# Optimization experiments

Hardware: AMD Instinct MI355X
Metric: run time of the kernel (lower is better)

Reference implementation:

```python
import jax, jax.numpy as jnp
import numpy as np

H_LSTM = 80          # span-encoder LSTM hidden
SPAN_DIM = 4 * H_LSTM  # 320
ADU_DIM = 256        # han_out_size
HEADS = 3
HAN_HID = 256
CTX_DIM = 200


def lstm(x, W_ih, W_hh, b, reverse=False):
    # x: [T, B, In] -> hidden states [T, B, H]; torch gate order i,f,g,o
    H = W_hh.shape[1]
    B = x.shape[1]

    def step(carry, xt):
        h, c = carry
        z = xt @ W_ih.T + h @ W_hh.T + b
        i, f, g, o = jnp.split(z, 4, axis=-1)
        c = jax.nn.sigmoid(f) * c + jax.nn.sigmoid(i) * jnp.tanh(g)
        h = jax.nn.sigmoid(o) * jnp.tanh(c)
        return (h, c), h

    init = (jnp.zeros((B, H), x.dtype), jnp.zeros((B, H), x.dtype))
    _, hs = jax.lax.scan(step, init, x, reverse=reverse)
    return hs


def span_rep(seq, spans):
    # seq [L, 2H], spans [..., 2] -> [..., 4H]
    f, bwd = seq[:, :H_LSTM], seq[:, H_LSTM:]
    i, j = spans[..., 0], spans[..., 1]
    fi1, fj = f[i - 1], f[j]
    bi, bj1 = bwd[i], bwd[j + 1]
    return jnp.concatenate([fj - fi1, bi - bj1, fi1, bj1], axis=-1)


def gat_metapath(h, src, dst, emask, W, a_l, a_r, bias):
    # single-metapath GATConv (dgl semantics): h [A, Din], W [K, Din, D]
    A = h.shape[0]
    hp = jnp.einsum('ad,kdo->ako', h, W)  # [A,K,D]
    e = jax.nn.leaky_relu(jnp.einsum('eko,ko->ek', hp[src], a_l)
                          + jnp.einsum('eko,ko->ek', hp[dst], a_r), 0.2)
    e = jnp.where(emask[:, None], e, -1e9)
    m = jax.ops.segment_max(e, dst, num_segments=A)           # [A,K]
    ex = jnp.where(emask[:, None], jnp.exp(e - m[dst]), 0.0)
    den = jax.ops.segment_sum(ex, dst, num_segments=A)
    alpha = ex / jnp.maximum(den[dst], 1e-9)                  # edge softmax per dst
    out = jax.ops.segment_sum(alpha[:, :, None] * hp[src], dst, num_segments=A)
    out = jax.nn.elu(out + bias)                              # [A,K,D]
    return out.reshape(A, -1)                                 # [A, K*D]


def attn_pool(feats, vals, mask, W1, b1, W2, b2):
    # tiny MLP -> Softmax over axis 0 over the kept (masked) set
    s = jnp.maximum(feats @ W1 + b1, 0.0) @ W2 + b2           # [N,1]
    s = jnp.where(mask[:, None], s, -1e9)
    a = jnp.where(mask[:, None], jax.nn.softmax(s, axis=0), 0.0)
    out = (a * vals).sum(0)
    return jnp.where(mask.any(), out, jnp.zeros_like(out))


def _forward(token_embed, info_scores,
             Wih_f, Whh_f, b_f, Wih_b, Whh_b, b_b,
             W_gat, a_l, a_r, b_gat, W_sem, b_sem, q_sem, W_pred, b_pred,
             W_adu1, b_adu1, W_adu2, b_adu2,
             W_inn1, b_inn1, W_inn2, b_inn2,
             W_int1, b_int1, W_int2, b_int2,
             Wih_c, Whh_c, b_c,
             comment_spans, adu_spans, adu_masks, local_masks,
             inner_src, inner_dst, inner_rel, inner_mask,
             inter_src, inter_dst, inter_rel, inter_mask):
    # bidirectional span encoder over frozen LF token embeddings
    x = token_embed.transpose(1, 0, 2)                        # [L, C, 768]
    hf = lstm(x, Wih_f, Whh_f, b_f)
    hb = lstm(x, Wih_b, Whh_b, b_b, reverse=True)
    span_enc = jnp.concatenate([hf, hb], -1).transpose(1, 0, 2)  # [C, L, 2H]

    def per_comment(seq, cspan, aspans, amask, lmask,
                    isrc, idst, irel, imask_e,
                    tsrc, tdst, trel, tmask_e, info):
        cemb = span_rep(seq, cspan)                           # [320]
        adus = span_rep(seq, aspans) * amask[:, None]         # [A, 320]
        A = adus.shape[0]
        # meta-paths: inner Attack, inner Support, inter AttackedBy(rev), inter SupportedBy(rev)
        srcs = jnp.stack([isrc, isrc, tdst, tdst])
        dsts = jnp.stack([idst, idst, tsrc, tsrc])
        masks = jnp.stack([imask_e & (irel == 0), imask_e & (irel == 1),
                           tmask_e & (trel == 0), tmask_e & (trel == 1)])
        z = jax.vmap(gat_metapath, in_axes=(None, 0, 0, 0, 0, 0, 0, 0))(
            adus, srcs, dsts, masks, W_gat, a_l, a_r, b_gat)  # [4, A, K*D]
        # semantic attention across meta-paths (masked mean over real nodes)
        w = jnp.tanh(z @ W_sem + b_sem) @ q_sem               # [4, A]
        w = (w * amask[None, :]).sum(1) / jnp.maximum(amask.sum(), 1)
        beta = jax.nn.softmax(w)                              # [4]
        zfin = jnp.einsum('m,mad->ad', beta, z)               # [A, K*D]
        adu_embeds = zfin @ W_pred + b_pred                   # [A, 256]
        # ADU attention pooling over locally-used ADUs
        feats = jnp.concatenate(
            [jnp.broadcast_to(cemb, (A, SPAN_DIM)), adu_embeds], -1)
        attended_adu = attn_pool(feats, adu_embeds, amask & lmask,
                                 W_adu1, b_adu1, W_adu2, b_adu2)

        def pair_attend(se, de, rel, me, W1, b1, W2, b2):
            # relation lut: Attack(0)->[0,1], Support(1)->[1,0]
            onehot = jnp.stack([rel, 1 - rel], -1).astype(adu_embeds.dtype)
            pe = jnp.concatenate([adu_embeds[se], adu_embeds[de], onehot], -1)  # [E,514]
            fp = jnp.concatenate(
                [jnp.broadcast_to(cemb, (pe.shape[0], SPAN_DIM)), pe], -1)
            return attn_pool(fp, pe, me, W1, b1, W2, b2)

        attended_inner = pair_attend(isrc, idst, irel, imask_e,
                                     W_inn1, b_inn1, W_inn2, b_inn2)
        # revert_inter_post_relations=True: embed = cat(emb[pair1], emb[pair0], rel)
        attended_inter = pair_attend(tdst, tsrc, trel, tmask_e,
                                     W_int1, b_int1, W_int2, b_int2)
        return jnp.concatenate([attended_adu, attended_inner, attended_inter,
                                info, cemb])                  # [1608]

    wo_ctx = jax.vmap(per_comment)(span_enc, comment_spans, adu_spans, adu_masks,
                                   local_masks, inner_src, inner_dst, inner_rel,
                                   inner_mask, inter_src, inter_dst, inter_rel,
                                   inter_mask, info_scores)   # [C, 1608]
    # comment compressor LSTM along the comment sequence (batch = 1)
    ctx = lstm(wo_ctx[:, None, :], Wih_c, Whh_c, b_c)[:, 0, :]  # [C, 200]
    return jnp.concatenate([ctx, wo_ctx], -1)                 # [C, 1808]


def setup_inputs():
    C, L, A, E, INFO = 64, 1024, 32, 48, 4
    key = jax.random.key(0)
    ks = iter(jax.random.split(key, 64))
    rng = np.random.default_rng(0)

    def u(shape):  # uniform init as in _weight_init, scaled for stability
        return jax.random.uniform(next(ks), shape, jnp.float32, -0.1, 0.1)

    token_embed = jax.random.normal(next(ks), (C, L, 768), jnp.float32)
    info_scores = jax.random.normal(next(ks), (C, INFO), jnp.float32)
    ci = rng.integers(1, L // 2, C)
    cj = rng.integers(L // 2, L - 2, C)
    comment_spans = jnp.stack([jnp.asarray(ci), jnp.asarray(cj)], 1).astype(jnp.int32)
    ai = rng.integers(1, L - 40, (C, A))
    adu_spans = jnp.stack([jnp.asarray(ai), jnp.asarray(ai + rng.integers(1, 30, (C, A)))], -1).astype(jnp.int32)
    adu_masks = jnp.ones((C, A), jnp.bool_)
    local_masks = jnp.asarray(rng.integers(0, 2, (C, A)) > 0)
    ei = lambda hi, shp: jnp.asarray(rng.integers(0, hi, shp), jnp.int32)
    eb = lambda shp: jnp.asarray(rng.integers(0, 2, shp) > 0)
    inp = dict(token_embed=token_embed, info_scores=info_scores,
               comment_spans=comment_spans, adu_spans=adu_spans,
               adu_masks=adu_masks, local_masks=local_masks,
               inner_src=ei(A, (C, E)), inner_dst=ei(A, (C, E)),
               inner_rel=ei(2, (C, E)), inner_mask=eb((C, E)),
               inter_src=ei(A, (C, E)), inter_dst=ei(A, (C, E)),
               inter_rel=ei(2, (C, E)), inter_mask=eb((C, E)))
    D_WO = SPAN_DIM + ADU_DIM * 5 + 4 + INFO  # 1608
    params = dict(
        Wih_f=u((4 * H_LSTM, 768)), Whh_f=u((4 * H_LSTM, H_LSTM)), b_f=u((4 * H_LSTM,)),
        Wih_b=u((4 * H_LSTM, 768)), Whh_b=u((4 * H_LSTM, H_LSTM)), b_b=u((4 * H_LSTM,)),
        W_gat=u((4, HEADS, SPAN_DIM, HAN_HID)), a_l=u((4, HEADS, HAN_HID)),
        a_r=u((4, HEADS, HAN_HID)), b_gat=u((4, HEADS, HAN_HID)),
        W_sem=u((HEADS * HAN_HID, 128)), b_sem=u((128,)), q_sem=u((128,)),
        W_pred=u((HEADS * HAN_HID, ADU_DIM)), b_pred=u((ADU_DIM,)),
        W_adu1=u((SPAN_DIM + ADU_DIM, 16)), b_adu1=u((16,)), W_adu2=u((16, 1)), b_adu2=u((1,)),
        W_inn1=u((SPAN_DIM + 2 * ADU_DIM + 2, 16)), b_inn1=u((16,)), W_inn2=u((16, 1)), b_inn2=u((1,)),
        W_int1=u((SPAN_DIM + 2 * ADU_DIM + 2, 16)), b_int1=u((16,)), W_int2=u((16, 1)), b_int2=u((1,)),
        Wih_c=u((4 * CTX_DIM, D_WO)), Whh_c=u((4 * CTX_DIM, CTX_DIM)), b_c=u((4 * CTX_DIM,)))
    inp.update(params)
    return inp


def reference(token_embed, info_scores,
              Wih_f, Whh_f, b_f, Wih_b, Whh_b, b_b,
              W_gat, a_l, a_r, b_gat, W_sem, b_sem, q_sem, W_pred, b_pred,
              W_adu1, b_adu1, W_adu2, b_adu2,
              W_inn1, b_inn1, W_inn2, b_inn2,
              W_int1, b_int1, W_int2, b_int2,
              Wih_c, Whh_c, b_c,
              comment_spans, adu_spans, adu_masks, local_masks,
              inner_src, inner_dst, inner_rel, inner_mask,
              inter_src, inter_dst, inter_rel, inter_mask):
    return _forward(token_embed, info_scores,
                    Wih_f, Whh_f, b_f, Wih_b, Whh_b, b_b,
                    W_gat, a_l, a_r, b_gat, W_sem, b_sem, q_sem, W_pred, b_pred,
                    W_adu1, b_adu1, W_adu2, b_adu2,
                    W_inn1, b_inn1, W_inn2, b_inn2,
                    W_int1, b_int1, W_int2, b_int2,
                    Wih_c, Whh_c, b_c,
                    comment_spans, adu_spans, adu_masks, local_masks,
                    inner_src, inner_dst, inner_rel, inner_mask,
                    inter_src, inter_dst, inter_rel, inter_mask)
```

## Files before the change

kernel.cpp:

```cpp
#include <hip/hip_runtime.h>
#include <hip/hip_bf16.h>
#include <hip/hip_fp16.h>
#include <stdint.h>

typedef unsigned int u32;
typedef unsigned short u16;
typedef __attribute__((ext_vector_type(8))) short short8;
typedef __attribute__((ext_vector_type(4))) float f32x4;
typedef _Float16 half2v __attribute__((ext_vector_type(2)));

#if defined(__has_builtin)
#if __has_builtin(__builtin_amdgcn_fdot2)
#define HAVE_FDOT2 1
#endif
#endif

__device__ __forceinline__ float bf2f_u(u32 lo16) { return __uint_as_float(lo16 << 16); }
__device__ __forceinline__ u32 f2bf_bits(float x) {
  u32 u = __float_as_uint(x);
  return (u + 0x7fffu + ((u >> 16) & 1u)) >> 16;
}
__device__ __forceinline__ u32 pk2bf(float x, float y) {
  return f2bf_bits(x) | (f2bf_bits(y) << 16);
}
__device__ __forceinline__ u32 pk2bf_tr(float x, float y) {
  return (__float_as_uint(y) & 0xffff0000u) | (__float_as_uint(x) >> 16);
}
__device__ __forceinline__ u32 pkh(float x, float y) {
  return (u32)__half_as_ushort(__float2half(x)) |
         ((u32)__half_as_ushort(__float2half(y)) << 16);
}
__device__ __forceinline__ float dot2h(u32 w, u32 h, float acc) {
#ifdef HAVE_FDOT2
  return __builtin_amdgcn_fdot2(__builtin_bit_cast(half2v, w), __builtin_bit_cast(half2v, h),
                                acc, false);
#else
  union { u32 u; __half2 h2; } uw, uh;
  uw.u = w; uh.u = h;
  float2 wf = __half22float2(uw.h2);
  float2 hf = __half22float2(uh.h2);
  return acc + wf.x * hf.x + wf.y * hf.y;
#endif
}
__device__ __forceinline__ float sigf(float x) { return 1.0f / (1.0f + __expf(-x)); }
__device__ __forceinline__ float tanhf_fast(float x) {
  float ax = fabsf(x);
  float e = __expf(-2.0f * ax);
  float t = (1.0f - e) / (1.0f + e);
  return x < 0.0f ? -t : t;
}
__device__ __forceinline__ float eluf(float x) { return x > 0.0f ? x : __expf(x) - 1.0f; }
__device__ __forceinline__ float lreluf(float x) { return x > 0.0f ? x : 0.2f * x; }

__device__ __forceinline__ int maskmode(const void* am) { return (*(const u32*)am) > 0xFFu; }
__device__ __forceinline__ int ldmask(const void* p, int i, int mb) {
  return mb ? (int)((const unsigned char*)p)[i] : ((const int*)p)[i];
}

__global__ void k_marker(float* out) { out[0] = 12345.0f; }

__global__ void k_prep(const float* __restrict__ Wgat, const float* __restrict__ al,
                       const float* __restrict__ ar, float* __restrict__ alproj,
                       float* __restrict__ arproj) {
  int idx = blockIdx.x * 256 + threadIdx.x;
  if (idx >= 3840) return;
  int mk = idx / 320, d = idx % 320;
  const float* wrow = Wgat + ((size_t)mk * 320 + d) * 256;
  const float* alp = al + mk * 256;
  const float* arp = ar + mk * 256;
  float sa = 0.f, sb = 0.f;
  for (int o = 0; o < 256; ++o) {
    float w = wrow[o];
    sa += w * alp[o];
    sb += w * arp[o];
  }
  alproj[idx] = sa;
  arproj[idx] = sb;
}

__global__ void k_pack(const float* __restrict__ whhc, uint4* __restrict__ wt4) {
  int idx = blockIdx.x * 256 + threadIdx.x;
  if (idx >= 20000) return;
  int k4 = idx / 800, r = idx % 800;
  const float* p = whhc + r * 200 + k4 * 8;
  wt4[idx] = (uint4){pkh(p[0], p[1]), pkh(p[2], p[3]), pkh(p[4], p[5]), pkh(p[6], p[7])};
}

__global__ __launch_bounds__(256) void k_gemm_in(
    const float* __restrict__ emb, const float* __restrict__ Wf, const float* __restrict__ Wb,
    const float* __restrict__ biasf, const float* __restrict__ biasb, float* __restrict__ Z) {
  __shared__ u16 Albs[128 * 40];
  __shared__ u16 Blbs[128 * 40];
  __shared__ float bias_l[128];
  const int tid = threadIdx.x;
  const int n0 = blockIdx.x * 128;
  const int m0 = blockIdx.y * 128;

  if (tid < 128) {
    int ng = n0 + tid;
    bias_l[tid] = (ng < 320) ? biasf[ng] : biasb[ng - 320];
  }

  const int srow = tid >> 1, shalf = tid & 1;
  const float* asrc = emb + (size_t)(m0 + srow) * 768 + shalf * 16;
  const int ngb = n0 + srow;
  const float* bsrc =
      ((ngb < 320) ? (Wf + (size_t)ngb * 768) : (Wb + (size_t)(ngb - 320) * 768)) + shalf * 16;
  u32* aw = (u32*)&Albs[srow * 40 + shalf * 16];
  u32* bw = (u32*)&Blbs[srow * 40 + shalf * 16];

  const int lane = tid & 63;
  const int lr = lane & 15, sub = lane >> 4;
  const int wv = tid >> 6, wm = wv >> 1, wn = wv & 1;
  const u16* abase = &Albs[(wm * 64 + lr) * 40 + sub * 8];
  const u16* bbase = &Blbs[(wn * 64 + lr) * 40 + sub * 8];

  f32x4 acc[4][4];
#pragma unroll
  for (int i = 0; i < 4; ++i)
#pragma unroll
    for (int j = 0; j < 4; ++j) acc[i][j] = (f32x4)(0.f);

  float4 a0, a1, a2, a3, b0, b1, b2, b3;
  u32 pra[8], prb[8];
  a0 = *(const float4*)(asrc + 0); a1 = *(const float4*)(asrc + 4);
  a2 = *(const float4*)(asrc + 8); a3 = *(const float4*)(asrc + 12);
  b0 = *(const float4*)(bsrc + 0); b1 = *(const float4*)(bsrc + 4);
  b2 = *(const float4*)(bsrc + 8); b3 = *(const float4*)(bsrc + 12);
  pra[0] = pk2bf_tr(a0.x, a0.y); pra[1] = pk2bf_tr(a0.z, a0.w);
  pra[2] = pk2bf_tr(a1.x, a1.y); pra[3] = pk2bf_tr(a1.z, a1.w);
  pra[4] = pk2bf_tr(a2.x, a2.y); pra[5] = pk2bf_tr(a2.z, a2.w);
  pra[6] = pk2bf_tr(a3.x, a3.y); pra[7] = pk2bf_tr(a3.z, a3.w);
  prb[0] = pk2bf_tr(b0.x, b0.y); prb[1] = pk2bf_tr(b0.z, b0.w);
  prb[2] = pk2bf_tr(b1.x, b1.y); prb[3] = pk2bf_tr(b1.z, b1.w);
  prb[4] = pk2bf_tr(b2.x, b2.y); prb[5] = pk2bf_tr(b2.z, b2.w);
  prb[6] = pk2bf_tr(b3.x, b3.y); prb[7] = pk2bf_tr(b3.z, b3.w);

  for (int it = 0; it < 24; ++it) {
    __syncthreads();
#pragma unroll
    for (int q = 0; q < 8; ++q) { aw[q] = pra[q]; bw[q] = prb[q]; }
    __syncthreads();
    const bool more = (it + 1 < 24);
    if (more) {
      const int k0 = (it + 1) * 32;
      a0 = *(const float4*)(asrc + k0); a1 = *(const float4*)(asrc + k0 + 4);
      a2 = *(const float4*)(asrc + k0 + 8); a3 = *(const float4*)(asrc + k0 + 12);
      b0 = *(const float4*)(bsrc + k0); b1 = *(const float4*)(bsrc + k0 + 4);
      b2 = *(const float4*)(bsrc + k0 + 8); b3 = *(const float4*)(bsrc + k0 + 12);
    }
    short8 bfr[4];
#pragma unroll
    for (int nf = 0; nf < 4; ++nf) bfr[nf] = *(const short8*)(bbase + nf * 640);
#pragma unroll
    for (int mf = 0; mf < 4; ++mf) {
      short8 af = *(const short8*)(abase + mf * 640);
#pragma unroll
      for (int nf = 0; nf < 4; ++nf)
        acc[mf][nf] = __builtin_amdgcn_mfma_f32_16x16x32_bf16(af, bfr[nf], acc[mf][nf], 0, 0, 0);
    }
    if (more) {
      pra[0] = pk2bf_tr(a0.x, a0.y); pra[1] = pk2bf_tr(a0.z, a0.w);
      pra[2] = pk2bf_tr(a1.x, a1.y); pra[3] = pk2bf_tr(a1.z, a1.w);
      pra[4] = pk2bf_tr(a2.x, a2.y); pra[5] = pk2bf_tr(a2.z, a2.w);
      pra[6] = pk2bf_tr(a3.x, a3.y); pra[7] = pk2bf_tr(a3.z, a3.w);
      prb[0] = pk2bf_tr(b0.x, b0.y); prb[1] = pk2bf_tr(b0.z, b0.w);
      prb[2] = pk2bf_tr(b1.x, b1.y); prb[3] = pk2bf_tr(b1.z, b1.w);
      prb[4] = pk2bf_tr(b2.x, b2.y); prb[5] = pk2bf_tr(b2.z, b2.w);
      prb[6] = pk2bf_tr(b3.x, b3.y); prb[7] = pk2bf_tr(b3.z, b3.w);
    }
  }

#pragma unroll
  for (int mf = 0; mf < 4; ++mf) {
#pragma unroll
    for (int nf = 0; nf < 4; ++nf) {
      int col = wn * 64 + nf * 16 + lr;
      float bias = bias_l[col];
      size_t mrow = (size_t)m0 + wm * 64 + mf * 16 + sub * 4;
#pragma unroll
      for (int j = 0; j < 4; ++j)
        Z[(mrow + j) * 640 + n0 + col] = acc[mf][nf][j] + bias;
    }
  }
}

__global__ __launch_bounds__(320, 1) void k_lstm_tok(const float* __restrict__ Z,
                                                     const float* __restrict__ Whhf,
                                                     const float* __restrict__ Whhb,
                                                     float* __restrict__ hf,
                                                     float* __restrict__ hb) {
  __shared__ uint2 wq[20 * 320];
  __shared__ alignas(16) u32 hpk[40];
  __shared__ float zbuf[320];
  const int tid = threadIdx.x;
  const int c = blockIdx.x >> 1;
  const int dir = blockIdx.x & 1;
  const float* Whh = dir ? Whhb : Whhf;
  float* hout = dir ? hb : hf;

  for (int idx = tid; idx < 20 * 320; idx += 320) {
    int k4 = idx / 320, r = idx % 320;
    const float* p = Whh + (size_t)r * 80 + k4 * 4;
    wq[idx] = (uint2){pkh(p[0], p[1]), pkh(p[2], p[3])};
  }
  if (tid < 40) hpk[tid] = 0;
  __syncthreads();

  const int j = tid;
  const uint2* wcol = wq + j;
  uint2 wv0 = wcol[0], wv1 = wcol[320], wv2 = wcol[640], wv3 = wcol[960];
  uint2 wv4 = wcol[1280], wv5 = wcol[1600], wv6 = wcol[1920], wv7 = wcol[2240];
  uint2 wv8 = wcol[2560], wv9 = wcol[2880], wv10 = wcol[3200], wv11 = wcol[3520];
  uint2 wv12 = wcol[3840], wv13 = wcol[4160], wv14 = wcol[4480], wv15 = wcol[4800];
  uint2 wv16 = wcol[5120], wv17 = wcol[5440], wv18 = wcol[5760], wv19 = wcol[6080];
  asm volatile("" : "+v"(wv0.x), "+v"(wv0.y), "+v"(wv1.x), "+v"(wv1.y), "+v"(wv2.x),
                    "+v"(wv2.y), "+v"(wv3.x), "+v"(wv3.y), "+v"(wv4.x), "+v"(wv4.y),
                    "+v"(wv5.x), "+v"(wv5.y), "+v"(wv6.x), "+v"(wv6.y), "+v"(wv7.x),
                    "+v"(wv7.y), "+v"(wv8.x), "+v"(wv8.y), "+v"(wv9.x), "+v"(wv9.y));
  asm volatile("" : "+v"(wv10.x), "+v"(wv10.y), "+v"(wv11.x), "+v"(wv11.y), "+v"(wv12.x),
                    "+v"(wv12.y), "+v"(wv13.x), "+v"(wv13.y), "+v"(wv14.x), "+v"(wv14.y),
                    "+v"(wv15.x), "+v"(wv15.y), "+v"(wv16.x), "+v"(wv16.y), "+v"(wv17.x),
                    "+v"(wv17.y), "+v"(wv18.x), "+v"(wv18.y), "+v"(wv19.x), "+v"(wv19.y));

  const int sgn = dir ? -1 : 1;
  const int t0 = dir ? 1023 : 0;
  const float* zb = Z + (size_t)c * 1024 * 640 + dir * 320 + j;
  float zc = zb[(size_t)t0 * 640];
  float zn = zb[(size_t)(t0 + sgn) * 640];
  float cst = 0.f;

  for (int t = 0; t < 1024; ++t) {
    const int tt = t0 + sgn * t;
    float zp = 0.f;
    if (t + 2 < 1024) zp = zb[(size_t)(t0 + sgn * (t + 2)) * 640];
    float a0 = zc, a1 = 0.f, a2 = 0.f, a3 = 0.f;
    {
      uint4 h0 = *(const uint4*)&hpk[0];
      a0 = dot2h(wv0.x, h0.x, a0); a1 = dot2h(wv0.y, h0.y, a1);
      a2 = dot2h(wv1.x, h0.z, a2); a3 = dot2h(wv1.y, h0.w, a3);
      uint4 h1 = *(const uint4*)&hpk[4];
      a0 = dot2h(wv2.x, h1.x, a0); a1 = dot2h(wv2.y, h1.y, a1);
      a2 = dot2h(wv3.x, h1.z, a2); a3 = dot2h(wv3.y, h1.w, a3);
      uint4 h2 = *(const uint4*)&hpk[8];
      a0 = dot2h(wv4.x, h2.x, a0); a1 = dot2h(wv4.y, h2.y, a1);
      a2 = dot2h(wv5.x, h2.z, a2); a3 = dot2h(wv5.y, h2.w, a3);
      uint4 h3 = *(const uint4*)&hpk[12];
      a0 = dot2h(wv6.x, h3.x, a0); a1 = dot2h(wv6.y, h3.y, a1);
      a2 = dot2h(wv7.x, h3.z, a2); a3 = dot2h(wv7.y, h3.w, a3);
      uint4 h4 = *(const uint4*)&hpk[16];
      a0 = dot2h(wv8.x, h4.x, a0); a1 = dot2h(wv8.y, h4.y, a1);
      a2 = dot2h(wv9.x, h4.z, a2); a3 = dot2h(wv9.y, h4.w, a3);
      uint4 h5 = *(const uint4*)&hpk[20];
      a0 = dot2h(wv10.x, h5.x, a0); a1 = dot2h(wv10.y, h5.y, a1);
      a2 = dot2h(wv11.x, h5.z, a2); a3 = dot2h(wv11.y, h5.w, a3);
      uint4 h6 = *(const uint4*)&hpk[24];
      a0 = dot2h(wv12.x, h6.x, a0); a1 = dot2h(wv12.y, h6.y, a1);
      a2 = dot2h(wv13.x, h6.z, a2); a3 = dot2h(wv13.y, h6.w, a3);
      uint4 h7 = *(const uint4*)&hpk[28];
      a0 = dot2h(wv14.x, h7.x, a0); a1 = dot2h(wv14.y, h7.y, a1);
      a2 = dot2h(wv15.x, h7.z, a2); a3 = dot2h(wv15.y, h7.w, a3);
      uint4 h8 = *(const uint4*)&hpk[32];
      a0 = dot2h(wv16.x, h8.x, a0); a1 = dot2h(wv16.y, h8.y, a1);
      a2 = dot2h(wv17.x, h8.z, a2); a3 = dot2h(wv17.y, h8.w, a3);
      uint4 h9 = *(const uint4*)&hpk[36];
      a0 = dot2h(wv18.x, h9.x, a0); a1 = dot2h(wv18.y, h9.y, a1);
      a2 = dot2h(wv19.x, h9.z, a2); a3 = dot2h(wv19.y, h9.w, a3);
    }
    zbuf[j] = (a0 + a1) + (a2 + a3);
    __syncthreads();
    if (j < 80) {
      float iv = sigf(zbuf[j]);
      float fv = sigf(zbuf[80 + j]);
      float gv = tanhf_fast(zbuf[160 + j]);
      float ov = sigf(zbuf[240 + j]);
      cst = fv * cst + iv * gv;
      float h = ov * tanhf_fast(cst);
      ((u16*)hpk)[j] = __half_as_ushort(__float2half(h));
      hout[((size_t)c * 1024 + tt) * 80 + j] = h;
    }
    zc = zn; zn = zp;
    __syncthreads();
  }
}

__device__ __forceinline__ float span_val(const float* __restrict__ hf,
                                          const float* __restrict__ hb, int c, int i, int j,
                                          int d) {
  size_t base = (size_t)c * 1024 * 80;
  if (d < 80) return hf[base + (size_t)j * 80 + d] - hf[base + (size_t)(i - 1) * 80 + d];
  if (d < 160) return hb[base + (size_t)i * 80 + (d - 80)] - hb[base + (size_t)(j + 1) * 80 + (d - 80)];
  if (d < 240) return hf[base + (size_t)(i - 1) * 80 + (d - 160)];
  return hb[base + (size_t)(j + 1) * 80 + (d - 240)];
}

__global__ __launch_bounds__(256) void k_span(const float* __restrict__ hf,
                                              const float* __restrict__ hb,
                                              const int* __restrict__ cspan,
                                              const int* __restrict__ aspan,
                                              const void* __restrict__ amask,
                                              float* __restrict__ adus, float* __restrict__ cembo) {
  const int c = blockIdx.x, tid = threadIdx.x;
  const int mb = maskmode(amask);
  int ci = cspan[c * 2], cj = cspan[c * 2 + 1];
  for (int d = tid; d < 320; d += 256) cembo[c * 320 + d] = span_val(hf, hb, c, ci, cj, d);
  for (int idx = tid; idx < 32 * 320; idx += 256) {
    int a = idx / 320, d = idx % 320;
    float v = 0.f;
    if (ldmask(amask, c * 32 + a, mb)) {
      int ai = aspan[(c * 32 + a) * 2], aj = aspan[(c * 32 + a) * 2 + 1];
      v = span_val(hf, hb, c, ai, aj, d);
    }
    adus[(size_t)c * 10240 + idx] = v;
  }
}

__global__ __launch_bounds__(256) void k_gat(
    const float* __restrict__ adus_ws, const float* __restrict__ alproj,
    const float* __restrict__ arproj, const float* __restrict__ Wgat,
    const float* __restrict__ bgat, const int* __restrict__ isrc, const int* __restrict__ idst,
    const int* __restrict__ irel, const void* __restrict__ imask, const int* __restrict__ tsrc,
    const int* __restrict__ tdst, const int* __restrict__ trel, const void* __restrict__ tmask,
    const void* __restrict__ amdet, float* __restrict__ zgat) {
  __shared__ float adus_l[32][321];
  __shared__ float Wst[16][64];
  __shared__ float hp_t[32][66];
  __shared__ float sl_l[96], sr_l[96];
  __shared__ float e_l[144], alpha_l[144], mx_l[96], den_l[96];
  __shared__ int src_l[48], dst_l[48], valid_l[48];
  const int c = blockIdx.x >> 2, m = blockIdx.x & 3;
  const int tid = threadIdx.x;
  const int mb = maskmode(amdet);

  if (tid < 48) {
    int e = tid, s, d, r, mk;
    if (m < 2) {
      s = isrc[c * 48 + e]; d = idst[c * 48 + e]; r = irel[c * 48 + e];
      mk = ldmask(imask, c * 48 + e, mb);
    } else {
      s = tdst[c * 48 + e]; d = tsrc[c * 48 + e]; r = trel[c * 48 + e];
      mk = ldmask(tmask, c * 48 + e, mb);
    }
    src_l[e] = s; dst_l[e] = d; valid_l[e] = (mk != 0) && (r == (m & 1));
  }
  for (int idx = tid; idx < 32 * 320; idx += 256)
    adus_l[idx / 320][idx % 320] = adus_ws[(size_t)c * 10240 + idx];
  __syncthreads();

  if (tid < 96) {
    int a = tid & 31, k = tid >> 5;
    const float* alp = alproj + (m * 3 + k) * 320;
    const float* arp = arproj + (m * 3 + k) * 320;
    float sa = 0.f, sb = 0.f;
    for (int d = 0; d < 320; ++d) {
      float v = adus_l[a][d];
      sa += v * alp[d];
      sb += v * arp[d];
    }
    sl_l[a * 3 + k] = sa;
    sr_l[a * 3 + k] = sb;
  }
  __syncthreads();
  if (tid < 144) {
    int e = tid % 48, k = tid / 48;
    float v = -1e30f;
    if (valid_l[e]) v = lreluf(sl_l[src_l[e] * 3 + k] + sr_l[dst_l[e] * 3 + k]);
    e_l[e * 3 + k] = v;
  }
  __syncthreads();
  if (tid < 96) {
    int a = tid & 31, k = tid >> 5;
    float mx = -1e30f;
    for (int e = 0; e < 48; ++e)
      if (valid_l[e] && dst_l[e] == a) mx = fmaxf(mx, e_l[e * 3 + k]);
    float den = 0.f;
    for (int e = 0; e < 48; ++e)
      if (valid_l[e] && dst_l[e] == a) den += __expf(e_l[e * 3 + k] - mx);
    mx_l[a * 3 + k] = mx;
    den_l[a * 3 + k] = den;
  }
  __syncthreads();
  if (tid < 144) {
    int e = tid % 48, k = tid / 48;
    float v = 0.f;
    if (valid_l[e]) {
      int d = dst_l[e];
      v = __expf(e_l[e * 3 + k] - mx_l[d * 3 + k]) / fmaxf(den_l[d * 3 + k], 1e-9f);
    }
    alpha_l[e * 3 + k] = v;
  }
  __syncthreads();

  const int ag = tid >> 3, og = tid & 7;
  for (int k = 0; k < 3; ++k) {
    for (int ot = 0; ot < 4; ++ot) {
      float acc[8];
#pragma unroll
      for (int i = 0; i < 8; ++i) acc[i] = 0.f;
      for (int dt = 0; dt < 320; dt += 16) {
        {
          int dd = tid >> 4, oq = (tid & 15) * 4;
          const float* p = Wgat + ((size_t)((m * 3 + k) * 320 + dt + dd)) * 256 + ot * 64 + oq;
          float4 v = *(const float4*)p;
          Wst[dd][oq + 0] = v.x;
          Wst[dd][oq + 1] = v.y;
          Wst[dd][oq + 2] = v.z;
          Wst[dd][oq + 3] = v.w;
        }
        __syncthreads();
#pragma unroll
        for (int dd = 0; dd < 16; ++dd) {
          float av = adus_l[ag][dt + dd];
          const float4 w0 = *(const float4*)(&Wst[dd][og * 8]);
          const float4 w1 = *(const float4*)(&Wst[dd][og * 8 + 4]);
          acc[0] += av * w0.x; acc[1] += av * w0.y; acc[2] += av * w0.z; acc[3] += av * w0.w;
          acc[4] += av * w1.x; acc[5] += av * w1.y; acc[6] += av * w1.z; acc[7] += av * w1.w;
        }
        __syncthreads();
      }
#pragma unroll
      for (int i = 0; i < 8; ++i) hp_t[ag][og * 8 + i] = acc[i];
      __syncthreads();
      float oacc[8];
#pragma unroll
      for (int i = 0; i < 8; ++i) oacc[i] = 0.f;
      for (int e = 0; e < 48; ++e) {
        if (valid_l[e] && dst_l[e] == ag) {
          float alv = alpha_l[e * 3 + k];
          int s = src_l[e];
#pragma unroll
          for (int i = 0; i < 8; ++i) oacc[i] += alv * hp_t[s][og * 8 + i];
        }
      }
#pragma unroll
      for (int i = 0; i < 8; ++i) {
        int o = ot * 64 + og * 8 + i;
        float v = eluf(oacc[i] + bgat[(m * 3 + k) * 256 + o]);
        zgat[((size_t)(c * 4 + m) * 32 + ag) * 768 + k * 256 + o] = v;
      }
      __syncthreads();
    }
  }
}

__global__ __launch_bounds__(256) void k_sem(const float* __restrict__ zgat,
                                             const float* __restrict__ Wsem,
                                             const float* __restrict__ bsem,
                                             const float* __restrict__ qsem,
                                             const void* __restrict__ amask,
                                             float* __restrict__ wsem) {
  __shared__ float Wst[64][128];
  __shared__ float zl[32][64];
  __shared__ float wred[256];
  __shared__ float war[32];
  const int c = blockIdx.x >> 2, m = blockIdx.x & 3;
  const int tid = threadIdx.x;
  const int mb = maskmode(amask);
  const int a = tid >> 3, hg = tid & 7;
  float acc[16];
#pragma unroll
  for (int i = 0; i < 16; ++i) acc[i] = 0.f;
  const float* zbase = zgat + (size_t)(c * 4 + m) * 32 * 768;
  for (int jt = 0; jt < 768; jt += 64) {
    for (int l = 0; l < 8; ++l) {
      int f4 = l * 256 + tid;
      int row = f4 >> 5, c4 = (f4 & 31) * 4;
      *(float4*)&Wst[row][c4] = *(const float4*)(Wsem + (size_t)(jt + row) * 128 + c4);
    }
    for (int l = 0; l < 2; ++l) {
      int f4 = l * 256 + tid;
      int row = f4 >> 4, c4 = (f4 & 15) * 4;
      *(float4*)&zl[row][c4] = *(const float4*)(zbase + (size_t)row * 768 + jt + c4);
    }
    __syncthreads();
    for (int j = 0; j < 64; ++j) {
      float zv = zl[a][j];
      const float* wp = &Wst[j][hg * 16];
#pragma unroll
      for (int i = 0; i < 16; ++i) acc[i] += zv * wp[i];
    }
    __syncthreads();
  }
  float wp_ = 0.f;
#pragma unroll
  for (int i = 0; i < 16; ++i) {
    int h = hg * 16 + i;
    wp_ += tanhf_fast(acc[i] + bsem[h]) * qsem[h];
  }
  wred[tid] = wp_;
  __syncthreads();
  if (tid < 32) {
    float s = 0.f;
    for (int q = 0; q < 8; ++q) s += wred[tid * 8 + q];
    war[tid] = s;
  }
  __syncthreads();
  if (tid == 0) {
    float s = 0.f;
    int cnt = 0;
    for (int aa = 0; aa < 32; ++aa)
      if (ldmask(amask, c * 32 + aa, mb)) { s += war[aa]; cnt++; }
    wsem[c * 4 + m] = s / (float)(cnt > 1 ? cnt : 1);
  }
}

__global__ __launch_bounds__(256) void k_comment(
    const float* __restrict__ zgat, const float* __restrict__ wsem,
    const float* __restrict__ cemb_ws, const float* __restrict__ Wpred,
    const float* __restrict__ bpred, const float* __restrict__ Wadu1,
    const float* __restrict__ badu1, const float* __restrict__ Wadu2,
    const float* __restrict__ badu2, const float* __restrict__ Winn1,
    const float* __restrict__ binn1, const float* __restrict__ Winn2,
    const float* __restrict__ binn2, const float* __restrict__ Wint1,
    const float* __restrict__ bint1, const float* __restrict__ Wint2,
    const float* __restrict__ bint2, const float* __restrict__ info,
    const void* __restrict__ amask, const void* __restrict__ lmask,
    const int* __restrict__ isrc, const int* __restrict__ idst,
    const int* __restrict__ irel, const void* __restrict__ imask, const int* __restrict__ tsrc,
    const int* __restrict__ tdst, const int* __restrict__ trel, const void* __restrict__ tmask,
    float* __restrict__ woctx, float* __restrict__ dout) {
  __shared__ float zf[32][133];
  __shared__ float ae[32][257];
  __shared__ float cemb_l[320];
  __shared__ float beta_l[4];
  __shared__ float pred_l[48][16];
  __shared__ float sE[48], alE[48];
  __shared__ int seL[48], deL[48], relL[48], mskL[48];
  __shared__ float wredA[256];
  __shared__ float sA[32], alA[32];
  __shared__ int mskA[32];
  const int c = blockIdx.x, tid = threadIdx.x;
  const int mb = maskmode(amask);

  if (tid == 0) {
    float w0 = wsem[c * 4], w1 = wsem[c * 4 + 1], w2 = wsem[c * 4 + 2], w3 = wsem[c * 4 + 3];
    float mx = fmaxf(fmaxf(w0, w1), fmaxf(w2, w3));
    float e0 = __expf(w0 - mx), e1 = __expf(w1 - mx), e2 = __expf(w2 - mx), e3 = __expf(w3 - mx);
    float s = e0 + e1 + e2 + e3;
    beta_l[0] = e0 / s; beta_l[1] = e1 / s; beta_l[2] = e2 / s; beta_l[3] = e3 / s;
  }
  for (int d = tid; d < 320; d += 256) cemb_l[d] = cemb_ws[c * 320 + d];
  __syncthreads();

  const int ag = tid >> 5;
  const int og = tid & 31;
  float acc[4][8];
#pragma unroll
  for (int i = 0; i < 4; ++i)
#pragma unroll
    for (int j = 0; j < 8; ++j) acc[i][j] = 0.f;
  const float b0 = beta_l[0], b1 = beta_l[1], b2 = beta_l[2], b3 = beta_l[3];
  const float* zc0 = zgat + (size_t)(c * 4 + 0) * 32 * 768;
  const float* zc1 = zgat + (size_t)(c * 4 + 1) * 32 * 768;
  const float* zc2 = zgat + (size_t)(c * 4 + 2) * 32 * 768;
  const float* zc3 = zgat + (size_t)(c * 4 + 3) * 32 * 768;
  for (int jt = 0; jt < 768; jt += 128) {
    for (int l = 0; l < 16; ++l) {
      int idx = l * 256 + tid;
      int a = idx >> 7, j = idx & 127;
      size_t off = (size_t)a * 768 + jt + j;
      zf[a][j] = b0 * zc0[off] + b1 * zc1[off] + b2 * zc2[off] + b3 * zc3[off];
    }
    __syncthreads();
    for (int j = 0; j < 128; ++j) {
      const float* wp = Wpred + (size_t)(jt + j) * 256 + og * 8;
      float4 w0v = *(const float4*)wp;
      float4 w1v = *(const float4*)(wp + 4);
      float w8[8] = {w0v.x, w0v.y, w0v.z, w0v.w, w1v.x, w1v.y, w1v.z, w1v.w};
      float z0 = zf[ag * 4 + 0][j], z1 = zf[ag * 4 + 1][j];
      float z2 = zf[ag * 4 + 2][j], z3 = zf[ag * 4 + 3][j];
#pragma unroll
      for (int jj = 0; jj < 8; ++jj) {
        acc[0][jj] += z0 * w8[jj];
        acc[1][jj] += z1 * w8[jj];
        acc[2][jj] += z2 * w8[jj];
        acc[3][jj] += z3 * w8[jj];
      }
    }
    __syncthreads();
  }
#pragma unroll
  for (int i = 0; i < 4; ++i)
#pragma unroll
    for (int jj = 0; jj < 8; ++jj)
      ae[ag * 4 + i][og * 8 + jj] = acc[i][jj] + bpred[og * 8 + jj];
  __syncthreads();

  {
    const int a = tid >> 3, hg = tid & 7;
    float sacc = 0.f;
    for (int hh = 0; hh < 2; ++hh) {
      int h = hg * 2 + hh;
      float d = badu1[h];
      for (int dd = 0; dd < 320; ++dd) d += cemb_l[dd] * Wadu1[dd * 16 + h];
      for (int dd = 0; dd < 256; ++dd) d += ae[a][dd] * Wadu1[(320 + dd) * 16 + h];
      sacc += fmaxf(d, 0.f) * Wadu2[h];
    }
    wredA[tid] = sacc;
  }
  __syncthreads();
  if (tid < 32) {
    float s = badu2[0];
    for (int q = 0; q < 8; ++q) s += wredA[tid * 8 + q];
    sA[tid] = s;
    mskA[tid] = (ldmask(amask, c * 32 + tid, mb) != 0) && (ldmask(lmask, c * 32 + tid, mb) != 0);
  }
  __syncthreads();
  if (tid == 0) {
    float mx = -1e30f;
    int any = 0;
    for (int a = 0; a < 32; ++a)
      if (mskA[a]) { any = 1; mx = fmaxf(mx, sA[a]); }
    float s = 0.f;
    for (int a = 0; a < 32; ++a) {
      float v = mskA[a] ? __expf(sA[a] - mx) : 0.f;
      alA[a] = v;
      s += v;
    }
    if (any)
      for (int a = 0; a < 32; ++a) alA[a] /= s;
  }
  __syncthreads();
  {
    int o = tid;
    float v = 0.f;
    for (int a = 0; a < 32; ++a) v += alA[a] * ae[a][o];
    woctx[c * 1608 + o] = v;
    dout[(size_t)c * 1808 + 200 + o] = v;
  }
  __syncthreads();

  for (int pp = 0; pp < 2; ++pp) {
    const float *W1, *b1v, *W2, *b2v;
    const int *seP, *deP, *relP;
    const void* mskP;
    int outoff;
    if (pp == 0) {
      W1 = Winn1; b1v = binn1; W2 = Winn2; b2v = binn2;
      seP = isrc; deP = idst; relP = irel; mskP = imask; outoff = 256;
    } else {
      W1 = Wint1; b1v = bint1; W2 = Wint2; b2v = bint2;
      seP = tdst; deP = tsrc; relP = trel; mskP = tmask; outoff = 770;
    }
    if (tid < 48) {
      seL[tid] = seP[c * 48 + tid];
      deL[tid] = deP[c * 48 + tid];
      relL[tid] = relP[c * 48 + tid];
      mskL[tid] = (ldmask(mskP, c * 48 + tid, mb) != 0);
    }
    __syncthreads();
    for (int u = tid; u < 768; u += 256) {
      int e = u >> 4, h = u & 15;
      int se = seL[e], de = deL[e];
      float rel = (float)relL[e];
      float d = b1v[h];
      for (int dd = 0; dd < 320; ++dd) d += cemb_l[dd] * W1[dd * 16 + h];
      for (int dd = 0; dd < 256; ++dd) d += ae[se][dd] * W1[(320 + dd) * 16 + h];
      for (int dd = 0; dd < 256; ++dd) d += ae[de][dd] * W1[(576 + dd) * 16 + h];
      d += rel * W1[832 * 16 + h] + (1.f - rel) * W1[833 * 16 + h];
      pred_l[e][h] = fmaxf(d, 0.f) * W2[h];
    }
    __syncthreads();
    if (tid < 48) {
      float s = b2v[0];
      for (int h = 0; h < 16; ++h) s += pred_l[tid][h];
      sE[tid] = s;
    }
    __syncthreads();
    if (tid == 0) {
      float mx = -1e30f;
      int any = 0;
      for (int e = 0; e < 48; ++e)
        if (mskL[e]) { any = 1; mx = fmaxf(mx, sE[e]); }
      float s = 0.f;
      for (int e = 0; e < 48; ++e) {
        float v = mskL[e] ? __expf(sE[e] - mx) : 0.f;
        alE[e] = v;
        s += v;
      }
      if (any)
        for (int e = 0; e < 48; ++e) alE[e] /= s;
    }
    __syncthreads();
    for (int dim = tid; dim < 514; dim += 256) {
      float v = 0.f;
      for (int e = 0; e < 48; ++e) {
        float alv = alE[e];
        float pe;
        if (dim < 256) pe = ae[seL[e]][dim];
        else if (dim < 512) pe = ae[deL[e]][dim - 256];
        else if (dim == 512) pe = (float)relL[e];
        else pe = 1.f - (float)relL[e];
        v += alv * pe;
      }
      woctx[c * 1608 + outoff + dim] = v;
      dout[(size_t)c * 1808 + 200 + outoff + dim] = v;
    }
    __syncthreads();
  }

  if (tid < 4) {
    float v = info[c * 4 + tid];
    woctx[c * 1608 + 1284 + tid] = v;
    dout[(size_t)c * 1808 + 200 + 1284 + tid] = v;
  }
  for (int d = tid; d < 320; d += 256) {
    float v = cemb_l[d];
    woctx[c * 1608 + 1288 + d] = v;
    dout[(size_t)c * 1808 + 200 + 1288 + d] = v;
  }
}

__global__ __launch_bounds__(256) void k_ctx_in(const float* __restrict__ woctx,
                                                const float* __restrict__ Wihc,
                                                const float* __restrict__ bc,
                                                float* __restrict__ xc) {
  __shared__ float woc[64][133];
  __shared__ float Wst[8][128];
  const int r0 = blockIdx.x * 8;
  const int tid = threadIdx.x;
  const int t = tid & 63, rg = tid >> 6;
  float a0 = 0.f, a1 = 0.f;
  for (int d0 = 0; d0 < 1608; d0 += 128) {
    int jn = 1608 - d0;
    if (jn > 128) jn = 128;
    for (int l = 0; l < 32; ++l) {
      int idx = l * 256 + tid;
      int tt = idx >> 7, j = idx & 127;
      woc[tt][j] = (j < jn) ? woctx[(size_t)tt * 1608 + d0 + j] : 0.f;
    }
    {
      int rr = tid >> 5, jb = tid & 31;
      for (int q = 0; q < 4; ++q) {
        int jj = jb * 4 + q;
        Wst[rr][jj] = (jj < jn) ? Wihc[(size_t)(r0 + rr) * 1608 + d0 + jj] : 0.f;
      }
    }
    __syncthreads();
    for (int j = 0; j < 128; ++j) {
      float x = woc[t][j];
      a0 += x * Wst[rg * 2 + 0][j];
      a1 += x * Wst[rg * 2 + 1][j];
    }
    __syncthreads();
  }
  int r = r0 + rg * 2;
  xc[t * 800 + r] = a0 + bc[r];
  xc[t * 800 + r + 1] = a1 + bc[r + 1];
}

__global__ __launch_bounds__(832) void k_ctx_rec(const float* __restrict__ xc,
                                                 const uint4* __restrict__ wt4,
                                                 float* __restrict__ dout) {
  __shared__ alignas(16) u32 hl2[100];
  __shared__ float zc[800];
  const int tid = threadIdx.x;
  if (tid < 100) hl2[tid] = 0;
  float cst = 0.f;
  __syncthreads();
  for (int t = 0; t < 64; ++t) {
    if (tid < 800) {
      float a0 = xc[t * 800 + tid], a1 = 0.f, a2 = 0.f, a3 = 0.f;
#pragma unroll 5
      for (int k4 = 0; k4 < 25; ++k4) {
        uint4 wv = wt4[(size_t)k4 * 800 + tid];
        uint4 hq = *(const uint4*)&hl2[k4 * 4];
        a0 = dot2h(wv.x, hq.x, a0);
        a1 = dot2h(wv.y, hq.y, a1);
        a2 = dot2h(wv.z, hq.z, a2);
        a3 = dot2h(wv.w, hq.w, a3);
      }
      zc[tid] = (a0 + a1) + (a2 + a3);
    }
    __syncthreads();
    if (tid < 200) {
      float iv = sigf(zc[tid]);
      float fv = sigf(zc[200 + tid]);
      float gv = tanhf_fast(zc[400 + tid]);
      float ov = sigf(zc[600 + tid]);
      cst = fv * cst + iv * gv;
      float h = ov * tanhf_fast(cst);
      ((u16*)hl2)[tid] = __half_as_ushort(__float2half(h));
      dout[(size_t)t * 1808 + tid] = h;
    }
    __syncthreads();
  }
}

extern "C" void kernel_launch(void* const* d_in, const int* in_sizes, int n_in, void* d_out,
                              int out_size, void* d_ws, size_t ws_size, hipStream_t stream) {
  const float* emb = (const float*)d_in[0];
  const float* info = (const float*)d_in[1];
  const int* cspan = (const int*)d_in[2];
  const int* aspan = (const int*)d_in[3];
  const void* amask = d_in[4];
  const void* lmask = d_in[5];
  const int* isrc = (const int*)d_in[6];
  const int* idst = (const int*)d_in[7];
  const int* irel = (const int*)d_in[8];
  const void* imask = d_in[9];
  const int* tsrc = (const int*)d_in[10];
  const int* tdst = (const int*)d_in[11];
  const int* trel = (const int*)d_in[12];
  const void* tmask = d_in[13];
  const float* Wihf = (const float*)d_in[14];
  const float* Whhf = (const float*)d_in[15];
  const float* bfv = (const float*)d_in[16];
  const float* Wihb = (const float*)d_in[17];
  const float* Whhb = (const float*)d_in[18];
  const float* bbv = (const float*)d_in[19];
  const float* Wgat = (const float*)d_in[20];
  const float* al = (const float*)d_in[21];
  const float* ar = (const float*)d_in[22];
  const float* bgat = (const float*)d_in[23];
  const float* Wsem = (const float*)d_in[24];
  const float* bsem = (const float*)d_in[25];
  const float* qsem = (const float*)d_in[26];
  const float* Wpred = (const float*)d_in[27];
  const float* bpred = (const float*)d_in[28];
  const float* Wadu1 = (const float*)d_in[29];
  const float* badu1 = (const float*)d_in[30];
  const float* Wadu2 = (const float*)d_in[31];
  const float* badu2 = (const float*)d_in[32];
  const float* Winn1 = (const float*)d_in[33];
  const float* binn1 = (const float*)d_in[34];
  const float* Winn2 = (const float*)d_in[35];
  const float* binn2 = (const float*)d_in[36];
  const float* Wint1 = (const float*)d_in[37];
  const float* bint1 = (const float*)d_in[38];
  const float* Wint2 = (const float*)d_in[39];
  const float* bint2 = (const float*)d_in[40];
  const float* Wihc = (const float*)d_in[41];
  const float* Whhc = (const float*)d_in[42];
  const float* bc = (const float*)d_in[43];
  float* out = (float*)d_out;
  float* ws = (float*)d_ws;

  const size_t OFF_Z = 0;
  const size_t OFF_HF = OFF_Z + (size_t)65536 * 640;
  const size_t OFF_HB = OFF_HF + (size_t)64 * 1024 * 80;
  const size_t OFF_ZG = OFF_HB + (size_t)64 * 1024 * 80;
  const size_t OFF_AD = OFF_ZG + (size_t)64 * 4 * 32 * 768;
  const size_t OFF_CE = OFF_AD + (size_t)64 * 32 * 320;
  const size_t OFF_WS4 = OFF_CE + 64 * 320;
  const size_t OFF_ALP = OFF_WS4 + 256;
  const size_t OFF_ARP = OFF_ALP + 3840;
  const size_t OFF_WO = OFF_ARP + 3840;
  const size_t OFF_XC = OFF_WO + (size_t)64 * 1608;
  const size_t OFF_WT = OFF_XC + (size_t)64 * 800;
  const size_t TOTAL = OFF_WT + 80000;

  if (n_in < 44 || ws_size < TOTAL * sizeof(float)) {
    k_marker<<<1, 1, 0, stream>>>(out);
    return;
  }

  k_prep<<<15, 256, 0, stream>>>(Wgat, al, ar, ws + OFF_ALP, ws + OFF_ARP);
  k_pack<<<79, 256, 0, stream>>>(Whhc, (uint4*)(ws + OFF_WT));
  dim3 g1(5, 512);
  k_gemm_in<<<g1, 256, 0, stream>>>(emb, Wihf, Wihb, bfv, bbv, ws + OFF_Z);
  k_lstm_tok<<<128, 320, 0, stream>>>(ws + OFF_Z, Whhf, Whhb, ws + OFF_HF, ws + OFF_HB);
  k_span<<<64, 256, 0, stream>>>(ws + OFF_HF, ws + OFF_HB, cspan, aspan, amask, ws + OFF_AD,
                                 ws + OFF_CE);
  k_gat<<<256, 256, 0, stream>>>(ws + OFF_AD, ws + OFF_ALP, ws + OFF_ARP, Wgat, bgat, isrc, idst,
                                 irel, imask, tsrc, tdst, trel, tmask, amask, ws + OFF_ZG);
  k_sem<<<256, 256, 0, stream>>>(ws + OFF_ZG, Wsem, bsem, qsem, amask, ws + OFF_WS4);
  k_comment<<<64, 256, 0, stream>>>(ws + OFF_ZG, ws + OFF_WS4, ws + OFF_CE, Wpred, bpred, Wadu1,
                                    badu1, Wadu2, badu2, Winn1, binn1, Winn2, binn2, Wint1, bint1,
                                    Wint2, bint2, info, amask, lmask, isrc, idst, irel, imask,
                                    tsrc, tdst, trel, tmask, ws + OFF_WO, out);
  k_ctx_in<<<100, 256, 0, stream>>>(ws + OFF_WO, Wihc, bc, ws + OFF_XC);
  k_ctx_rec<<<1, 832, 0, stream>>>(ws + OFF_XC, (const uint4*)(ws + OFF_WT), out);
}
```

Measured before the change: 1.849 ms.

## Prepack GEMM inputs to bf16 and make LSTM step use shuffles with double-buffered state

Adds separate kernels that convert the token embeddings and input weights to bf16 once, plus a GEMM variant that loads those packed operands directly. The variant runs only when the workspace is large enough. The token LSTM now assigns the four gates of each hidden unit to adjacent lanes, gathers them with wave shuffles, and double-buffers the packed hidden state. This drops one of the two block barriers per timestep. The costs are an extra pass over the full embedding tensor and a larger workspace requirement.

```diff
diff --git a/kernel.cpp b/kernel.cpp
--- a/kernel.cpp
+++ b/kernel.cpp
@@ -86,6 +86,25 @@
   wt4[idx] = (uint4){pkh(p[0], p[1]), pkh(p[2], p[3]), pkh(p[4], p[5]), pkh(p[6], p[7])};
 }
 
+__global__ void k_packemb(const float* __restrict__ emb, u32* __restrict__ dst) {
+  const float4* s = (const float4*)emb;
+  uint2* d = (uint2*)dst;
+  const int n = 12582912;
+  for (int i = blockIdx.x * blockDim.x + threadIdx.x; i < n; i += gridDim.x * blockDim.x) {
+    float4 v = s[i];
+    d[i] = (uint2){pk2bf_tr(v.x, v.y), pk2bf_tr(v.z, v.w)};
+  }
+}
+
+__global__ void k_packw(const float* __restrict__ Wf, const float* __restrict__ Wb,
+                        u32* __restrict__ dst) {
+  int idx = blockIdx.x * 256 + threadIdx.x;
+  if (idx >= 245760) return;
+  int n = idx / 384, q = (idx % 384) * 2;
+  const float* src = (n < 320) ? (Wf + (size_t)n * 768) : (Wb + (size_t)(n - 320) * 768);
+  dst[idx] = pk2bf_tr(src[q], src[q + 1]);
+}
+
 __global__ __launch_bounds__(256) void k_gemm_in(
     const float* __restrict__ emb, const float* __restrict__ Wf, const float* __restrict__ Wb,
     const float* __restrict__ biasf, const float* __restrict__ biasb, float* __restrict__ Z) {
@@ -100,7 +119,6 @@
     int ng = n0 + tid;
     bias_l[tid] = (ng < 320) ? biasf[ng] : biasb[ng - 320];
   }
-
   const int srow = tid >> 1, shalf = tid & 1;
   const float* asrc = emb + (size_t)(m0 + srow) * 768 + shalf * 16;
   const int ngb = n0 + srow;
@@ -170,7 +188,73 @@
       prb[6] = pk2bf_tr(b3.x, b3.y); prb[7] = pk2bf_tr(b3.z, b3.w);
     }
   }
-
+#pragma unroll
+  for (int mf = 0; mf < 4; ++mf) {
+#pragma unroll
+    for (int nf = 0; nf < 4; ++nf) {
+      int col = wn * 64 + nf * 16 + lr;
+      float bias = bias_l[col];
+      size_t mrow = (size_t)m0 + wm * 64 + mf * 16 + sub * 4;
+#pragma unroll
+      for (int j = 0; j < 4; ++j)
+        Z[(mrow + j) * 640 + n0 + col] = acc[mf][nf][j] + bias;
+    }
+  }
+}
+
+__global__ __launch_bounds__(256) void k_gemm_in2(
+    const u32* __restrict__ ebf, const u32* __restrict__ wbf, const float* __restrict__ biasf,
+    const float* __restrict__ biasb, float* __restrict__ Z) {
+  __shared__ u16 Albs[128 * 40];
+  __shared__ u16 Blbs[128 * 40];
+  __shared__ float bias_l[128];
+  const int tid = threadIdx.x;
+  const int n0 = blockIdx.x * 128;
+  const int m0 = blockIdx.y * 128;
+
+  if (tid < 128) {
+    int ng = n0 + tid;
+    bias_l[tid] = (ng < 320) ? biasf[ng] : biasb[ng - 320];
+  }
+  const int srow = tid >> 1, shalf = tid & 1;
+  const uint4* ea = (const uint4*)ebf + (size_t)(m0 + srow) * 96 + shalf * 2;
+  const uint4* eb = (const uint4*)wbf + (size_t)(n0 + srow) * 96 + shalf * 2;
+  uint4* aw4 = (uint4*)&Albs[srow * 40 + shalf * 16];
+  uint4* bw4 = (uint4*)&Blbs[srow * 40 + shalf * 16];
+
+  const int lane = tid & 63;
+  const int lr = lane & 15, sub = lane >> 4;
+  const int wv = tid >> 6, wm = wv >> 1, wn = wv & 1;
+  const u16* abase = &Albs[(wm * 64 + lr) * 40 + sub * 8];
+  const u16* bbase = &Blbs[(wn * 64 + lr) * 40 + sub * 8];
+
+  f32x4 acc[4][4];
+#pragma unroll
+  for (int i = 0; i < 4; ++i)
+#pragma unroll
+    for (int j = 0; j < 4; ++j) acc[i][j] = (f32x4)(0.f);
+
+  uint4 pa0 = ea[0], pa1 = ea[1], pb0 = eb[0], pb1 = eb[1];
+  for (int it = 0; it < 24; ++it) {
+    __syncthreads();
+    aw4[0] = pa0; aw4[1] = pa1;
+    bw4[0] = pb0; bw4[1] = pb1;
+    __syncthreads();
+    if (it + 1 < 24) {
+      pa0 = ea[(it + 1) * 4]; pa1 = ea[(it + 1) * 4 + 1];
+      pb0 = eb[(it + 1) * 4]; pb1 = eb[(it + 1) * 4 + 1];
+    }
+    short8 bfr[4];
+#pragma unroll
+    for (int nf = 0; nf < 4; ++nf) bfr[nf] = *(const short8*)(bbase + nf * 640);
+#pragma unroll
+    for (int mf = 0; mf < 4; ++mf) {
+      short8 af = *(const short8*)(abase + mf * 640);
+#pragma unroll
+      for (int nf = 0; nf < 4; ++nf)
+        acc[mf][nf] = __builtin_amdgcn_mfma_f32_16x16x32_bf16(af, bfr[nf], acc[mf][nf], 0, 0, 0);
+    }
+  }
 #pragma unroll
   for (int mf = 0; mf < 4; ++mf) {
 #pragma unroll
@@ -191,8 +275,8 @@
                                                      float* __restrict__ hf,
                                                      float* __restrict__ hb) {
   __shared__ uint2 wq[20 * 320];
-  __shared__ alignas(16) u32 hpk[40];
-  __shared__ float zbuf[320];
+  __shared__ alignas(16) u32 hpkA[40];
+  __shared__ alignas(16) u32 hpkB[40];
   const int tid = threadIdx.x;
   const int c = blockIdx.x >> 1;
   const int dir = blockIdx.x & 1;
@@ -204,11 +288,13 @@
     const float* p = Whh + (size_t)r * 80 + k4 * 4;
     wq[idx] = (uint2){pkh(p[0], p[1]), pkh(p[2], p[3])};
   }
-  if (tid < 40) hpk[tid] = 0;
-  __syncthreads();
-
-  const int j = tid;
-  const uint2* wcol = wq + j;
+  if (tid < 40) hpkA[tid] = 0;
+  __syncthreads();
+
+  const int u = tid >> 2, g = tid & 3;
+  const int r = g * 80 + u;
+  const int lb = tid & 60;
+  const uint2* wcol = wq + r;
   uint2 wv0 = wcol[0], wv1 = wcol[320], wv2 = wcol[640], wv3 = wcol[960];
   uint2 wv4 = wcol[1280], wv5 = wcol[1600], wv6 = wcol[1920], wv7 = wcol[2240];
   uint2 wv8 = wcol[2560], wv9 = wcol[2880], wv10 = wcol[3200], wv11 = wcol[3520];
@@ -225,10 +311,13 @@
 
   const int sgn = dir ? -1 : 1;
   const int t0 = dir ? 1023 : 0;
-  const float* zb = Z + (size_t)c * 1024 * 640 + dir * 320 + j;
+  const float* zb = Z + (size_t)c * 1024 * 640 + dir * 320 + r;
   float zc = zb[(size_t)t0 * 640];
   float zn = zb[(size_t)(t0 + sgn) * 640];
   float cst = 0.f;
+  const u32* cur = hpkA;
+  u32* nxt = hpkB;
+  float* hbase = hout + (size_t)c * 1024 * 80 + u;
 
   for (int t = 0; t < 1024; ++t) {
     const int tt = t0 + sgn * t;
@@ -236,50 +325,54 @@
     if (t + 2 < 1024) zp = zb[(size_t)(t0 + sgn * (t + 2)) * 640];
     float a0 = zc, a1 = 0.f, a2 = 0.f, a3 = 0.f;
     {
-      uint4 h0 = *(const uint4*)&hpk[0];
+      uint4 h0 = *(const uint4*)&cur[0];
       a0 = dot2h(wv0.x, h0.x, a0); a1 = dot2h(wv0.y, h0.y, a1);
       a2 = dot2h(wv1.x, h0.z, a2); a3 = dot2h(wv1.y, h0.w, a3);
-      uint4 h1 = *(const uint4*)&hpk[4];
+      uint4 h1 = *(const uint4*)&cur[4];
       a0 = dot2h(wv2.x, h1.x, a0); a1 = dot2h(wv2.y, h1.y, a1);
       a2 = dot2h(wv3.x, h1.z, a2); a3 = dot2h(wv3.y, h1.w, a3);
-      uint4 h2 = *(const uint4*)&hpk[8];
+      uint4 h2 = *(const uint4*)&cur[8];
       a0 = dot2h(wv4.x, h2.x, a0); a1 = dot2h(wv4.y, h2.y, a1);
       a2 = dot2h(wv5.x, h2.z, a2); a3 = dot2h(wv5.y, h2.w, a3);
-      uint4 h3 = *(const uint4*)&hpk[12];
+      uint4 h3 = *(const uint4*)&cur[12];
       a0 = dot2h(wv6.x, h3.x, a0); a1 = dot2h(wv6.y, h3.y, a1);
       a2 = dot2h(wv7.x, h3.z, a2); a3 = dot2h(wv7.y, h3.w, a3);
-      uint4 h4 = *(const uint4*)&hpk[16];
+      uint4 h4 = *(const uint4*)&cur[16];
       a0 = dot2h(wv8.x, h4.x, a0); a1 = dot2h(wv8.y, h4.y, a1);
       a2 = dot2h(wv9.x, h4.z, a2); a3 = dot2h(wv9.y, h4.w, a3);
-      uint4 h5 = *(const uint4*)&hpk[20];
+      uint4 h5 = *(const uint4*)&cur[20];
       a0 = dot2h(wv10.x, h5.x, a0); a1 = dot2h(wv10.y, h5.y, a1);
       a2 = dot2h(wv11.x, h5.z, a2); a3 = dot2h(wv11.y, h5.w, a3);
-      uint4 h6 = *(const uint4*)&hpk[24];
+      uint4 h6 = *(const uint4*)&cur[24];
       a0 = dot2h(wv12.x, h6.x, a0); a1 = dot2h(wv12.y, h6.y, a1);
       a2 = dot2h(wv13.x, h6.z, a2); a3 = dot2h(wv13.y, h6.w, a3);
-      uint4 h7 = *(const uint4*)&hpk[28];
+      uint4 h7 = *(const uint4*)&cur[28];
       a0 = dot2h(wv14.x, h7.x, a0); a1 = dot2h(wv14.y, h7.y, a1);
       a2 = dot2h(wv15.x, h7.z, a2); a3 = dot2h(wv15.y, h7.w, a3);
-      uint4 h8 = *(const uint4*)&hpk[32];
+      uint4 h8 = *(const uint4*)&cur[32];
       a0 = dot2h(wv16.x, h8.x, a0); a1 = dot2h(wv16.y, h8.y, a1);
       a2 = dot2h(wv17.x, h8.z, a2); a3 = dot2h(wv17.y, h8.w, a3);
-      uint4 h9 = *(const uint4*)&hpk[36];
+      uint4 h9 = *(const uint4*)&cur[36];
       a0 = dot2h(wv18.x, h9.x, a0); a1 = dot2h(wv18.y, h9.y, a1);
       a2 = dot2h(wv19.x, h9.z, a2); a3 = dot2h(wv19.y, h9.w, a3);
     }
-    zbuf[j] = (a0 + a1) + (a2 + a3);
-    __syncthreads();
-    if (j < 80) {
-      float iv = sigf(zbuf[j]);
-      float fv = sigf(zbuf[80 + j]);
-      float gv = tanhf_fast(zbuf[160 + j]);
-      float ov = sigf(zbuf[240 + j]);
-      cst = fv * cst + iv * gv;
-      float h = ov * tanhf_fast(cst);
-      ((u16*)hpk)[j] = __half_as_ushort(__float2half(h));
-      hout[((size_t)c * 1024 + tt) * 80 + j] = h;
+    float asum = (a0 + a1) + (a2 + a3);
+    float zi = __shfl(asum, lb + 0, 64);
+    float zf_ = __shfl(asum, lb + 1, 64);
+    float zg = __shfl(asum, lb + 2, 64);
+    float zo = __shfl(asum, lb + 3, 64);
+    float iv = sigf(zi);
+    float fv = sigf(zf_);
+    float gv = tanhf_fast(zg);
+    float ov = sigf(zo);
+    cst = fv * cst + iv * gv;
+    float h = ov * tanhf_fast(cst);
+    if (g == 0) {
+      ((u16*)nxt)[u] = (u16)__half_as_ushort(__float2half(h));
+      hbase[(size_t)tt * 80] = h;
     }
     zc = zn; zn = zp;
+    const u32* tc = cur; cur = nxt; nxt = (u32*)tc;
     __syncthreads();
   }
 }
@@ -849,16 +942,27 @@
   const size_t OFF_XC = OFF_WO + (size_t)64 * 1608;
   const size_t OFF_WT = OFF_XC + (size_t)64 * 800;
   const size_t TOTAL = OFF_WT + 80000;
+  const size_t OFF_EBF = TOTAL;
+  const size_t OFF_WBF = OFF_EBF + (size_t)65536 * 384;
+  const size_t TOTAL_EXT = OFF_WBF + 245760;
 
   if (n_in < 44 || ws_size < TOTAL * sizeof(float)) {
     k_marker<<<1, 1, 0, stream>>>(out);
     return;
   }
+  const bool ext = ws_size >= TOTAL_EXT * sizeof(float);
 
   k_prep<<<15, 256, 0, stream>>>(Wgat, al, ar, ws + OFF_ALP, ws + OFF_ARP);
   k_pack<<<79, 256, 0, stream>>>(Whhc, (uint4*)(ws + OFF_WT));
   dim3 g1(5, 512);
-  k_gemm_in<<<g1, 256, 0, stream>>>(emb, Wihf, Wihb, bfv, bbv, ws + OFF_Z);
+  if (ext) {
+    k_packemb<<<2048, 256, 0, stream>>>(emb, (u32*)(ws + OFF_EBF));
+    k_packw<<<960, 256, 0, stream>>>(Wihf, Wihb, (u32*)(ws + OFF_WBF));
+    k_gemm_in2<<<g1, 256, 0, stream>>>((const u32*)(ws + OFF_EBF), (const u32*)(ws + OFF_WBF),
+                                       bfv, bbv, ws + OFF_Z);
+  } else {
+    k_gemm_in<<<g1, 256, 0, stream>>>(emb, Wihf, Wihb, bfv, bbv, ws + OFF_Z);
+  }
   k_lstm_tok<<<128, 320, 0, stream>>>(ws + OFF_Z, Whhf, Whhb, ws + OFF_HF, ws + OFF_HB);
   k_span<<<64, 256, 0, stream>>>(ws + OFF_HF, ws + OFF_HB, cspan, aspan, amask, ws + OFF_AD,
                                  ws + OFF_CE);
```

New measurement: 1.909 ms. 1.03x slower.
